# Performance work log

Hardware: AMD Instinct MI355X
Metric: run time of the kernel (lower is better)

## Reference

```python
import jax, jax.numpy as jnp
import numpy as np
import math

# dims
B, DM, H, W = 8, 256, 32, 32
R = 4                      # num_rotations
DI = 2 * DM                # d_inner = expand * d_model = 512
DH = DI // 2               # 256
N = 16                     # d_state
K = 4                      # d_conv
DTR = math.ceil(DM / 16)   # dt_rank = 16


def _dwconv1d(x, w, b):
    # x: (B, C, L); w: (C, 1, K); torch padding='same' (even kernel: extra pad on right)
    lo = (K - 1) // 2
    y = jax.lax.conv_general_dilated(x, w, (1,), [(lo, K - 1 - lo)],
                                     dimension_numbers=('NCH', 'OIH', 'NCH'),
                                     feature_group_count=x.shape[1])
    return y + b[None, :, None]


def _conv2d(x, w, b=None, pad=0):
    y = jax.lax.conv_general_dilated(x, w, (1, 1), [(pad, pad), (pad, pad)],
                                     dimension_numbers=('NCHW', 'OIHW', 'NCHW'))
    return y if b is None else y + b[None, :, None, None]


def _selective_scan(u, delta, A, Bm, Cm):
    # u, delta: (b,r,d,l); A: (r,d,n); Bm, Cm: (b,r,n,l)
    xs = (jnp.moveaxis(delta, -1, 0), jnp.moveaxis(u, -1, 0),
          jnp.moveaxis(Bm, -1, 0), jnp.moveaxis(Cm, -1, 0))
    h0 = jnp.zeros(u.shape[:3] + (A.shape[-1],), u.dtype)  # (b,r,d,n)
    def step(h, inp):
        dt, ut, bt, ct = inp
        h = jnp.exp(dt[..., None] * A) * h + (dt * ut)[..., None] * bt[:, :, None, :]
        return h, jnp.einsum('brdn,brn->brd', h, ct)
    _, ys = jax.lax.scan(step, h0, xs)
    return jnp.moveaxis(ys, 0, -1)  # (b,r,d,l)


def setup_inputs() -> dict:
    key = jax.random.key(0)
    ks = iter(jax.random.split(key, 32))
    def rn(shape, s=0.02):
        return jax.random.normal(next(ks), shape, jnp.float32) * s
    return {
        'x': jax.random.normal(next(ks), (B, DM, H, W), jnp.float32),
        'in_proj_w': rn((DI, DM)),
        'out_proj_w': rn((DM, DI)),
        'conv_x_w': rn((R * DH, 1, K), 0.1), 'conv_x_b': rn((R * DH,), 0.1),
        'conv_z_w': rn((R * DH, 1, K), 0.1), 'conv_z_b': rn((R * DH,), 0.1),
        'x_proj_weight': rn((R, DTR + 2 * N, DH)),
        'dt_projs_weight': jax.random.uniform(next(ks), (R, DH, DTR)) * 0.1,
        'dt_projs_bias': jax.random.uniform(next(ks), (R, DH)) * 0.1,
        'A_logs': jax.random.normal(next(ks), (R * DH, N)) * 0.5,
        'Ds': jnp.ones((R * DH,), jnp.float32),
        'sa_w1': rn((DI // 4, R * DI, 3, 3)), 'sa_b1': jnp.zeros((DI // 4,)),
        'sa_w2': rn((R, DI // 4, 1, 1)), 'sa_b2': jnp.zeros((R,)),
        'ca_w1': rn((DI // 16, R * DI, 1, 1)),
        'ca_w2': rn((R, DI // 16, 1, 1)),
        'gate_w': rn((DI, 2 * DI, 1, 1)), 'gate_b': jnp.zeros((DI,)),
    }


def reference(x, in_proj_w, out_proj_w, conv_x_w, conv_x_b, conv_z_w, conv_z_b,
              x_proj_weight, dt_projs_weight, dt_projs_bias, A_logs, Ds,
              sa_w1, sa_b1, sa_w2, sa_b2, ca_w1, ca_w2, gate_w, gate_b):
    b = x.shape[0]
    L = H * W
    # in_proj (1x1 conv), then 4 rotations (first='l')
    xz = jnp.einsum('bchw,dc->bdhw', x, in_proj_w)                      # (b,DI,H,W)
    xz_rot = jnp.stack([jnp.rot90(xz, r, axes=(2, 3)) for r in range(R)], axis=1)
    xh, zh = jnp.split(xz_rot, 2, axis=2)                               # (b,R,DH,H,W)
    x_seq = jax.nn.silu(_dwconv1d(xh.reshape(b, R * DH, L), conv_x_w, conv_x_b))
    z_seq = jax.nn.silu(_dwconv1d(zh.reshape(b, R * DH, L), conv_z_w, conv_z_b))
    x4 = x_seq.reshape(b, R, DH, L)
    # input-dependent SSM params
    x_dbl = jnp.einsum('brdl,rkd->brkl', x4, x_proj_weight)
    dts, Bm, Cm = jnp.split(x_dbl, [DTR, DTR + N], axis=2)
    delta = jnp.einsum('brkl,rdk->brdl', dts, dt_projs_weight)
    delta = jax.nn.softplus(delta + dt_projs_bias[None, :, :, None])
    A = -jnp.exp(A_logs).reshape(R, DH, N)
    y = _selective_scan(x4, delta, A, Bm, Cm)
    y = y + Ds.reshape(R, DH)[None, :, :, None] * x4
    # MambaVision-style: concat scan output with gated z branch -> d_inner
    y = jnp.concatenate([y, z_seq.reshape(b, R, DH, L)], axis=2).reshape(b, R, DI, H, W)
    # undo rotations so branches are spatially aligned
    y = jnp.stack([jnp.rot90(y[:, r], -r, axes=(2, 3)) for r in range(R)], axis=1)
    # hybrid RotationAwareFusion
    y_flat = y.reshape(b, R * DI, H, W)
    sw = jax.nn.relu(_conv2d(y_flat, sa_w1, sa_b1, pad=1))
    sw = jax.nn.softmax(_conv2d(sw, sa_w2, sa_b2), axis=1)              # (b,R,H,W)
    spatial = jnp.einsum('brchw,brhw->bchw', y, sw)
    cavg = y.mean(axis=(3, 4)).reshape(b, R * DI, 1, 1)
    cw = jax.nn.relu(_conv2d(cavg, ca_w1))
    cw = jax.nn.softmax(_conv2d(cw, ca_w2), axis=1)[:, :, 0, 0]         # (b,R)
    channel = jnp.einsum('brchw,br->bchw', y, cw)
    g = jax.nn.sigmoid(_conv2d(jnp.concatenate([spatial, channel], axis=1), gate_w, gate_b))
    fused = g * spatial + (1.0 - g) * channel                           # (b,DI,H,W)
    out = jnp.einsum('bdhw,cd->bchw', fused, out_proj_w)
    return jax.nn.gelu(out)
```

## Files before the change

kernel.cpp:

```cpp
#include <hip/hip_runtime.h>
#include <math.h>


typedef _Float16 half8 __attribute__((ext_vector_type(8)));
typedef float f4 __attribute__((ext_vector_type(4)));

__device__ __forceinline__ int srcmap(int r, int l) {
  int i = l >> 5, j = l & 31;
  int h, w;
  if (r == 0)      { h = i;      w = j;      }
  else if (r == 1) { h = j;      w = 31 - i; }
  else if (r == 2) { h = 31 - i; w = 31 - j; }
  else             { h = 31 - j; w = i;      }
  return (h << 5) + w;
}

__device__ __forceinline__ float siluf(float x)    { return x / (1.f + __expf(-x)); }
__device__ __forceinline__ float sigmoidf_(float x){ return 1.f / (1.f + __expf(-x)); }
__device__ __forceinline__ float geluf(float x) {
  float x3 = x * x * x;
  return 0.5f * x * (1.f + tanhf(0.7978845608028654f * (x + 0.044715f * x3)));
}

__global__ void k_prep(const float* __restrict__ inw, const float* __restrict__ gw,
                       const float* __restrict__ opw,
                       float* __restrict__ inWT, _Float16* __restrict__ gwH,
                       _Float16* __restrict__ opH) {
  int idx = blockIdx.x * 256 + threadIdx.x;
  if (idx < 131072) {
    int c = idx >> 9, d = idx & 511;
    inWT[idx] = inw[d * 256 + c];
  } else if (idx < 655360) {
    int i = idx - 131072;
    gwH[i] = (_Float16)gw[i];
  } else {
    int i = idx - 655360;
    opH[i] = (_Float16)opw[i];
  }
}

__global__ void k_wprep(const float* __restrict__ saw1, _Float16* __restrict__ Whg2) {
  int o = blockIdx.x * 256 + threadIdx.x;
  int ci = o & 2047;
  int co = (o >> 11) & 127;
  int tap = o >> 18;
  size_t dst = (((size_t)(tap * 64 + (ci >> 5)) * 128) + co) * 32 + (ci & 31);
  Whg2[dst] = (_Float16)saw1[((size_t)co * 2048 + ci) * 9 + tap];
}

__global__ void __launch_bounds__(512) k_inproj(const float* __restrict__ x,
                                                const float* __restrict__ inWT,
                                                float* __restrict__ xz) {
  int d = threadIdx.x;
  int b = blockIdx.y;
  int p0 = blockIdx.x * 16;
  const float* xb = x + (size_t)(b * 256) * 1024 + p0;
  float acc[16];
#pragma unroll
  for (int j = 0; j < 16; ++j) acc[j] = 0.f;
  for (int c = 0; c < 256; ++c) {
    float w = inWT[c * 512 + d];
    const float* xr = xb + c * 1024;
#pragma unroll
    for (int q = 0; q < 4; ++q) {
      float4 v = *(const float4*)(xr + q * 4);
      acc[q*4+0] = fmaf(w, v.x, acc[q*4+0]);
      acc[q*4+1] = fmaf(w, v.y, acc[q*4+1]);
      acc[q*4+2] = fmaf(w, v.z, acc[q*4+2]);
      acc[q*4+3] = fmaf(w, v.w, acc[q*4+3]);
    }
  }
  float* o = xz + (size_t)(b * 512 + d) * 1024 + p0;
#pragma unroll
  for (int q = 0; q < 4; ++q) {
    float4 ov = {acc[q*4+0], acc[q*4+1], acc[q*4+2], acc[q*4+3]};
    *(float4*)(o + q * 4) = ov;
  }
}

__global__ void __launch_bounds__(256) k_conv(const float* __restrict__ xz,
                                              const float* __restrict__ cxw,
                                              const float* __restrict__ cxb,
                                              const float* __restrict__ czw,
                                              const float* __restrict__ czb,
                                              float* __restrict__ xseq,
                                              float* __restrict__ Y) {
  int d = blockIdx.x;
  int b = blockIdx.y;
  __shared__ float xs_t[1024];
  __shared__ float zs_t[1024];
  int t4 = threadIdx.x * 4;
  *(float4*)&xs_t[t4] = *(const float4*)(xz + ((size_t)(b * 512 + d)) * 1024 + t4);
  *(float4*)&zs_t[t4] = *(const float4*)(xz + ((size_t)(b * 512 + 256 + d)) * 1024 + t4);
  __syncthreads();
#pragma unroll
  for (int r = 0; r < 4; ++r) {
    int rd = r * 256 + d;
    float xw0 = cxw[rd*4+0], xw1 = cxw[rd*4+1], xw2 = cxw[rd*4+2], xw3 = cxw[rd*4+3];
    float zw0 = czw[rd*4+0], zw1 = czw[rd*4+1], zw2 = czw[rd*4+2], zw3 = czw[rd*4+3];
    float xbi = cxb[rd], zbi = czb[rd];
    float xo[4], zo[4];
#pragma unroll
    for (int q = 0; q < 4; ++q) {
      int l = t4 + q;
      float ax = xbi, az = zbi;
      if (l - 1 >= 0) {
        int s = srcmap(r, l - 1);
        ax = fmaf(xw0, xs_t[s], ax); az = fmaf(zw0, zs_t[s], az);
      }
      {
        int s = srcmap(r, l);
        ax = fmaf(xw1, xs_t[s], ax); az = fmaf(zw1, zs_t[s], az);
      }
      if (l + 1 < 1024) {
        int s = srcmap(r, l + 1);
        ax = fmaf(xw2, xs_t[s], ax); az = fmaf(zw2, zs_t[s], az);
      }
      if (l + 2 < 1024) {
        int s = srcmap(r, l + 2);
        ax = fmaf(xw3, xs_t[s], ax); az = fmaf(zw3, zs_t[s], az);
      }
      xo[q] = siluf(ax); zo[q] = siluf(az);
    }
    *(float4*)(xseq + ((size_t)(b * 4 + r) * 256 + d) * 1024 + t4) = *(float4*)xo;
    *(float4*)(Y + ((size_t)(b * 4 + r) * 512 + 256 + d) * 1024 + t4) = *(float4*)zo;
  }
}

__global__ void __launch_bounds__(256) k_xdblT(const float* __restrict__ xseq,
                                               const float* __restrict__ xpw,
                                               float* __restrict__ xdT) {
  int ch = blockIdx.x;
  int br = blockIdx.y;
  int r  = br & 3;
  __shared__ float xs_t[256][33];
  const float* base = xseq + (size_t)(br * 256) * 1024 + ch * 32;
  {
    int c4 = threadIdx.x & 7;
    int drow = threadIdx.x >> 3;
#pragma unroll
    for (int p = 0; p < 8; ++p) {
      int dd = p * 32 + drow;
      float4 v = *(const float4*)(base + (size_t)dd * 1024 + c4 * 4);
      xs_t[dd][c4*4+0] = v.x; xs_t[dd][c4*4+1] = v.y;
      xs_t[dd][c4*4+2] = v.z; xs_t[dd][c4*4+3] = v.w;
    }
  }
  __syncthreads();
  int c  = threadIdx.x & 31;
  int kq = threadIdx.x >> 5;
  const float* w = xpw + (r * 48 + kq * 6) * 256;
  float acc[6] = {0.f, 0.f, 0.f, 0.f, 0.f, 0.f};
  for (int d0 = 0; d0 < 256; d0 += 4) {
    float x0 = xs_t[d0][c], x1 = xs_t[d0+1][c], x2 = xs_t[d0+2][c], x3 = xs_t[d0+3][c];
#pragma unroll
    for (int j = 0; j < 6; ++j) {
      float4 wv = *(const float4*)(w + j * 256 + d0);
      acc[j] = fmaf(wv.x, x0, fmaf(wv.y, x1, fmaf(wv.z, x2, fmaf(wv.w, x3, acc[j]))));
    }
  }
  float* o = xdT + ((size_t)(br * 32 + ch) * 32 + c) * 48 + kq * 6;
#pragma unroll
  for (int j = 0; j < 6; ++j) o[j] = acc[j];
}

__global__ void __launch_bounds__(256) k_scanA(
    const float* __restrict__ xseq, const float* __restrict__ xdT,
    const float* __restrict__ dtw_, const float* __restrict__ dtb_,
    const float* __restrict__ alogs,
    float* __restrict__ aprodg, float* __restrict__ Yc) {
  int ch = blockIdx.x;
  int br = blockIdx.y; int r = br & 3;
  int d  = threadIdx.x;
  int rd = r * 256 + d;
  f4 w0 = *(const f4*)&dtw_[rd * 16], w1 = *(const f4*)&dtw_[rd * 16 + 4],
     w2 = *(const f4*)&dtw_[rd * 16 + 8], w3 = *(const f4*)&dtw_[rd * 16 + 12];
  float A2[16], h[16], ap[16];
#pragma unroll
  for (int n = 0; n < 16; ++n) A2[n] = -__expf(alogs[rd * 16 + n]) * 1.44269504f;
#pragma unroll
  for (int n = 0; n < 16; ++n) { h[n] = 0.f; ap[n] = 1.f; }
  float bias = dtb_[rd];
  __shared__ __align__(16) float t2[1536];
  const float* xd = xdT + (size_t)(br * 32 + ch) * 1536;
  for (int i = threadIdx.x; i < 384; i += 256) ((f4*)t2)[i] = ((const f4*)xd)[i];
  __syncthreads();
  const float* us = xseq + (size_t)(br * 256 + d) * 1024 + ch * 32;
  for (int c4 = 0; c4 < 8; ++c4) {
    float4 uv = *(const float4*)(us + c4 * 4);
    float uarr[4] = {uv.x, uv.y, uv.z, uv.w};
#pragma unroll
    for (int cc = 0; cc < 4; ++cc) {
      const f4* row = (const f4*)&t2[(c4 * 4 + cc) * 48];
      f4 td0 = row[0], td1 = row[1], td2 = row[2], td3 = row[3];
      float delta = bias
        + td0[0]*w0[0] + td0[1]*w0[1] + td0[2]*w0[2] + td0[3]*w0[3]
        + td1[0]*w1[0] + td1[1]*w1[1] + td1[2]*w1[2] + td1[3]*w1[3]
        + td2[0]*w2[0] + td2[1]*w2[1] + td2[2]*w2[2] + td2[3]*w2[3]
        + td3[0]*w3[0] + td3[1]*w3[1] + td3[2]*w3[2] + td3[3]*w3[3];
      float sp = (delta > 20.f) ? delta : __logf(1.f + __expf(delta));
      float du = sp * uarr[cc];
      f4 tb[4] = {row[4], row[5], row[6], row[7]};
#pragma unroll
      for (int n = 0; n < 16; ++n) {
        float e = exp2f(sp * A2[n]);
        h[n] = fmaf(e, h[n], du * tb[n >> 2][n & 3]);
        ap[n] *= e;
      }
    }
  }
  float* apo = aprodg + ((size_t)(br * 32 + ch) * 256 + d) * 16;
  float* hco = Yc + (size_t)(br * 512 + d) * 1024 + ch * 32;
#pragma unroll
  for (int n = 0; n < 16; ++n) { apo[n] = ap[n]; hco[n] = h[n]; }
}

__global__ void k_scanB(const float* __restrict__ aprodg, float* __restrict__ Yc) {
  int t  = blockIdx.x * 256 + threadIdx.x;
  int br = t >> 12;
  int dn = t & 4095;
  int d = dn >> 4, n = dn & 15;
  float h = 0.f;
  for (int c = 0; c < 32; ++c) {
    size_t ao = (size_t)(br * 32 + c) * 4096 + dn;
    size_t yo = (size_t)(br * 512 + d) * 1024 + c * 32 + n;
    float hin = h;
    h = fmaf(aprodg[ao], h, Yc[yo]);
    Yc[yo] = hin;
  }
}

__global__ void __launch_bounds__(256) k_scanC(
    const float* __restrict__ xseq, const float* __restrict__ xdT,
    const float* __restrict__ dtw_, const float* __restrict__ dtb_,
    const float* __restrict__ alogs, const float* __restrict__ ds_,
    float* __restrict__ Y) {
  int ch = blockIdx.x;
  int br = blockIdx.y; int r = br & 3;
  int d  = threadIdx.x;
  int rd = r * 256 + d;
  f4 w0 = *(const f4*)&dtw_[rd * 16], w1 = *(const f4*)&dtw_[rd * 16 + 4],
     w2 = *(const f4*)&dtw_[rd * 16 + 8], w3 = *(const f4*)&dtw_[rd * 16 + 12];
  float A2[16], h[16];
#pragma unroll
  for (int n = 0; n < 16; ++n) A2[n] = -__expf(alogs[rd * 16 + n]) * 1.44269504f;
  float bias = dtb_[rd];
  float dsv  = ds_[rd];
  __shared__ __align__(16) float t2[1536];
  __shared__ float yt[32][257];
  const float* xd = xdT + (size_t)(br * 32 + ch) * 1536;
  for (int i = threadIdx.x; i < 384; i += 256) ((f4*)t2)[i] = ((const f4*)xd)[i];
  float* ybase = Y + (size_t)(br * 512 + d) * 1024 + ch * 32;
#pragma unroll
  for (int n = 0; n < 16; ++n) h[n] = ybase[n];
  __syncthreads();
  const float* us = xseq + (size_t)(br * 256 + d) * 1024 + ch * 32;
  for (int c4 = 0; c4 < 8; ++c4) {
    float4 uv = *(const float4*)(us + c4 * 4);
    float uarr[4] = {uv.x, uv.y, uv.z, uv.w};
#pragma unroll
    for (int cc = 0; cc < 4; ++cc) {
      int c = c4 * 4 + cc;
      const f4* row = (const f4*)&t2[c * 48];
      f4 td0 = row[0], td1 = row[1], td2 = row[2], td3 = row[3];
      float delta = bias
        + td0[0]*w0[0] + td0[1]*w0[1] + td0[2]*w0[2] + td0[3]*w0[3]
        + td1[0]*w1[0] + td1[1]*w1[1] + td1[2]*w1[2] + td1[3]*w1[3]
        + td2[0]*w2[0] + td2[1]*w2[1] + td2[2]*w2[2] + td2[3]*w2[3]
        + td3[0]*w3[0] + td3[1]*w3[1] + td3[2]*w3[2] + td3[3]*w3[3];
      float sp = (delta > 20.f) ? delta : __logf(1.f + __expf(delta));
      float du = sp * uarr[cc];
      f4 tb[4] = {row[4], row[5], row[6], row[7]};
      f4 tc[4] = {row[8], row[9], row[10], row[11]};
      float acc = 0.f;
#pragma unroll
      for (int n = 0; n < 16; ++n) {
        float e = exp2f(sp * A2[n]);
        h[n] = fmaf(e, h[n], du * tb[n >> 2][n & 3]);
        acc  = fmaf(h[n], tc[n >> 2][n & 3], acc);
      }
      yt[c][d] = fmaf(dsv, uarr[cc], acc);
    }
  }
  __syncthreads();
  for (int i = threadIdx.x; i < 2048; i += 256) {
    int dd = i >> 3, lq = i & 7;
    f4 v = {yt[lq * 4 + 0][dd], yt[lq * 4 + 1][dd], yt[lq * 4 + 2][dd], yt[lq * 4 + 3][dd]};
    *(f4*)(Y + (size_t)(br * 512 + dd) * 1024 + ch * 32 + lq * 4) = v;
  }
}

__global__ void k_ytr(const float* __restrict__ Y, _Float16* __restrict__ Ytg) {
  __shared__ float t[32][132];
  int l0  = blockIdx.x * 128;
  int ci0 = blockIdx.y * 32;
  int b   = blockIdx.z;
  int r   = ci0 >> 9;
  const float* src = Y + ((size_t)(b * 2048 + ci0)) * 1024 + l0;
#pragma unroll
  for (int i = 0; i < 16; ++i) {
    int idx = threadIdx.x + i * 256;
    int ci = idx >> 7, pp = idx & 127;
    t[ci][pp] = src[(size_t)ci * 1024 + pp];
  }
  __syncthreads();
  int pp = threadIdx.x >> 1;
  int ch = (threadIdx.x & 1) * 16;
  _Float16 buf[16];
#pragma unroll
  for (int j = 0; j < 16; ++j) buf[j] = (_Float16)t[ch + j][pp];
  int pix = srcmap(r, l0 + pp);
  _Float16* dst = Ytg + ((size_t)(b * 1024) + pix) * 2048 + ci0 + ch;
  *(float4*)dst = *(const float4*)buf;
  *(float4*)(dst + 8) = *(const float4*)(buf + 8);
}

__global__ void __launch_bounds__(256, 2) k_samfma(const _Float16* __restrict__ Ytg,
                                                   const _Float16* __restrict__ Whg2,
                                                   float* __restrict__ cpart) {
  __shared__ __align__(16) _Float16 As[6][32][40];
  __shared__ __align__(16) _Float16 Bs[9][64][40];
  int L = blockIdx.x;
  int ks = L & 7;
  int rem = L >> 3;
  int b = rem >> 3, rg = rem & 7;
  int tid = threadIdx.x;
  int wid = tid >> 6, lane = tid & 63;
  int r = lane & 15, g = lane >> 4;
  const _Float16* Yb = Ytg + (size_t)b * (1024 * 2048);
  const half8 zero8 = {0, 0, 0, 0, 0, 0, 0, 0};

  int srow[3], scol[3], sci8[3], srcoff[3]; bool sok[3];
#pragma unroll
  for (int i = 0; i < 3; ++i) {
    int unit = tid + i * 256;
    srow[i] = unit >> 7; scol[i] = (unit >> 2) & 31; sci8[i] = unit & 3;
    int grow = rg * 4 - 1 + srow[i];
    sok[i] = ((unsigned)grow < 32u);
    srcoff[i] = ((sok[i] ? grow : 0) * 32 + scol[i]) * 2048 + sci8[i] * 8;
  }
  int bcol = tid >> 2, bci8 = tid & 3;
  int ci_base = ks * 256;

  for (int coh = 0; coh < 2; ++coh) {
    f4 acc[2][4];
#pragma unroll
    for (int mi = 0; mi < 2; ++mi)
#pragma unroll
      for (int ni = 0; ni < 4; ++ni) acc[mi][ni] = (f4){0.f, 0.f, 0.f, 0.f};

    half8 pa[3], pb[9];
#pragma unroll
    for (int i = 0; i < 3; ++i) {
      half8 v = *(const half8*)(Yb + srcoff[i] + ci_base);
      pa[i] = sok[i] ? v : zero8;
    }
#pragma unroll
    for (int j = 0; j < 9; ++j)
      pb[j] = *(const half8*)(Whg2 + (((size_t)(j * 64 + ks * 8) * 128) + coh * 64 + bcol) * 32 + bci8 * 8);

    for (int ch = 0; ch < 8; ++ch) {
      __syncthreads();
#pragma unroll
      for (int i = 0; i < 3; ++i)
        *(half8*)&As[srow[i]][scol[i]][sci8[i] * 8] = pa[i];
#pragma unroll
      for (int j = 0; j < 9; ++j)
        *(half8*)&Bs[j][bcol][bci8 * 8] = pb[j];
      if (ch < 7) {
        int ci0 = ci_base + (ch + 1) * 32;
#pragma unroll
        for (int i = 0; i < 3; ++i) {
          half8 v = *(const half8*)(Yb + srcoff[i] + ci0);
          pa[i] = sok[i] ? v : zero8;
        }
        int cic = ks * 8 + ch + 1;
#pragma unroll
        for (int j = 0; j < 9; ++j)
          pb[j] = *(const half8*)(Whg2 + (((size_t)(j * 64 + cic) * 128) + coh * 64 + bcol) * 32 + bci8 * 8);
      }
      __syncthreads();

#pragma unroll
      for (int tap = 0; tap < 9; ++tap) {
        const int dh = tap / 3 - 1, dw = tap % 3 - 1;
        int lrow = wid + dh + 1;
        half8 av[2], bv[4];
#pragma unroll
        for (int mi = 0; mi < 2; ++mi) {
          int lcol = mi * 16 + r + dw;
          bool ok = ((unsigned)lcol < 32u);
          half8 v = *(const half8*)&As[lrow][lcol & 31][g * 8];
          av[mi] = ok ? v : zero8;
        }
#pragma unroll
        for (int ni = 0; ni < 4; ++ni)
          bv[ni] = *(const half8*)&Bs[tap][ni * 16 + r][g * 8];
#pragma unroll
        for (int mi = 0; mi < 2; ++mi)
#pragma unroll
          for (int ni = 0; ni < 4; ++ni)
            acc[mi][ni] = __builtin_amdgcn_mfma_f32_16x16x32_f16(av[mi], bv[ni], acc[mi][ni], 0, 0, 0);
      }
    }

    float* cp = cpart + (size_t)ks * (8192 * 128);
    int basepix = b * 1024 + (rg * 4 + wid) * 32;
#pragma unroll
    for (int mi = 0; mi < 2; ++mi)
#pragma unroll
      for (int ni = 0; ni < 4; ++ni) {
        int co = coh * 64 + ni * 16 + r;
#pragma unroll
        for (int j = 0; j < 4; ++j)
          cp[(size_t)(basepix + mi * 16 + g * 4 + j) * 128 + co] = acc[mi][ni][j];
      }
    __syncthreads();
  }
}

__global__ void __launch_bounds__(256) k_saconv2f(const float* __restrict__ cpart,
                                                  const float* __restrict__ sab1,
                                                  const float* __restrict__ saw2,
                                                  const float* __restrict__ sab2,
                                                  float* __restrict__ swout) {
  int tid = threadIdx.x;
  int pixg = tid >> 3, cig = tid & 7;
  int p = blockIdx.x * 32 + pixg;
  int b = blockIdx.y;
  int pix = b * 1024 + p;
  const float* c0 = cpart + (size_t)pix * 128 + cig * 16;
  float a0 = 0.f, a1 = 0.f, a2 = 0.f, a3 = 0.f;
#pragma unroll
  for (int j4 = 0; j4 < 4; ++j4) {
    float sx = 0.f, sy = 0.f, sz = 0.f, sw_ = 0.f;
#pragma unroll
    for (int k = 0; k < 8; ++k) {
      float4 v = *(const float4*)(c0 + (size_t)k * 1048576 + j4 * 4);
      sx += v.x; sy += v.y; sz += v.z; sw_ += v.w;
    }
    int ci = cig * 16 + j4 * 4;
    float v0 = fmaxf(sx + sab1[ci],     0.f);
    float v1 = fmaxf(sy + sab1[ci + 1], 0.f);
    float v2 = fmaxf(sz + sab1[ci + 2], 0.f);
    float v3 = fmaxf(sw_ + sab1[ci + 3], 0.f);
    a0 = fmaf(v0, saw2[ci], fmaf(v1, saw2[ci+1], fmaf(v2, saw2[ci+2], fmaf(v3, saw2[ci+3], a0))));
    a1 = fmaf(v0, saw2[128+ci], fmaf(v1, saw2[128+ci+1], fmaf(v2, saw2[128+ci+2], fmaf(v3, saw2[128+ci+3], a1))));
    a2 = fmaf(v0, saw2[256+ci], fmaf(v1, saw2[256+ci+1], fmaf(v2, saw2[256+ci+2], fmaf(v3, saw2[256+ci+3], a2))));
    a3 = fmaf(v0, saw2[384+ci], fmaf(v1, saw2[384+ci+1], fmaf(v2, saw2[384+ci+2], fmaf(v3, saw2[384+ci+3], a3))));
  }
#pragma unroll
  for (int off = 4; off > 0; off >>= 1) {
    a0 += __shfl_down(a0, off, 8);
    a1 += __shfl_down(a1, off, 8);
    a2 += __shfl_down(a2, off, 8);
    a3 += __shfl_down(a3, off, 8);
  }
  if (cig == 0) {
    a0 += sab2[0]; a1 += sab2[1]; a2 += sab2[2]; a3 += sab2[3];
    float m = fmaxf(fmaxf(a0, a1), fmaxf(a2, a3));
    float e0 = __expf(a0 - m), e1 = __expf(a1 - m), e2 = __expf(a2 - m), e3 = __expf(a3 - m);
    float inv = 1.f / (e0 + e1 + e2 + e3);
    swout[(b * 4 + 0) * 1024 + p] = e0 * inv;
    swout[(b * 4 + 1) * 1024 + p] = e1 * inv;
    swout[(b * 4 + 2) * 1024 + p] = e2 * inv;
    swout[(b * 4 + 3) * 1024 + p] = e3 * inv;
  }
}

__global__ void k_cavg(const float* __restrict__ Y, float* __restrict__ cavg) {
  int gidq = blockIdx.x * 256 + threadIdx.x;
  int row = gidq >> 2, q = gidq & 3;
  const float4* yr = (const float4*)(Y + (size_t)row * 1024 + q * 256);
  float s = 0.f;
  for (int i = 0; i < 64; ++i) {
    float4 v = yr[i];
    s += v.x + v.y + v.z + v.w;
  }
  s += __shfl_down(s, 2, 4);
  s += __shfl_down(s, 1, 4);
  if (q == 0) cavg[row] = s * (1.f / 1024.f);
}

__global__ void k_cw(const float* __restrict__ cavg, const float* __restrict__ caw1,
                     const float* __restrict__ caw2, float* __restrict__ cwout) {
  int b = blockIdx.x;
  int t = threadIdx.x;
  __shared__ float hid[32];
  __shared__ float vv[4];
  if (t < 32) {
    float a = 0.f;
    const float* cv = cavg + b * 2048;
    const float* wr = caw1 + t * 2048;
    for (int i = 0; i < 2048; ++i) a = fmaf(wr[i], cv[i], a);
    hid[t] = fmaxf(a, 0.f);
  }
  __syncthreads();
  if (t < 4) {
    float a = 0.f;
    for (int i = 0; i < 32; ++i) a = fmaf(caw2[t * 32 + i], hid[i], a);
    vv[t] = a;
  }
  __syncthreads();
  if (t < 4) {
    float m = fmaxf(fmaxf(vv[0], vv[1]), fmaxf(vv[2], vv[3]));
    float e = __expf(vv[t] - m);
    float s = __expf(vv[0] - m) + __expf(vv[1] - m) + __expf(vv[2] - m) + __expf(vv[3] - m);
    cwout[b * 4 + t] = e / s;
  }
}

__global__ void __launch_bounds__(256) k_catH(const _Float16* __restrict__ Ytg,
                                              const float* __restrict__ swv,
                                              const float* __restrict__ cwv,
                                              _Float16* __restrict__ catO) {
  int p0 = blockIdx.x * 64, c0 = blockIdx.y * 64, b = blockIdx.z;
  int pp = threadIdx.x >> 2, cs = (threadIdx.x & 3) * 16;
  int pix = p0 + pp;
  const _Float16* src = Ytg + (size_t)(b * 1024 + pix) * 2048 + c0 + cs;
  float accS[16], accC[16];
#pragma unroll
  for (int j = 0; j < 16; ++j) { accS[j] = 0.f; accC[j] = 0.f; }
#pragma unroll
  for (int r = 0; r < 4; ++r) {
    half8 v0 = *(const half8*)(src + r * 512);
    half8 v1 = *(const half8*)(src + r * 512 + 8);
    float sw = swv[(size_t)(b * 4 + r) * 1024 + pix];
    float cw = cwv[b * 4 + r];
#pragma unroll
    for (int j = 0; j < 8; ++j) {
      float f0 = (float)v0[j], f1 = (float)v1[j];
      accS[j]     = fmaf(f0, sw, accS[j]);
      accS[j + 8] = fmaf(f1, sw, accS[j + 8]);
      accC[j]     = fmaf(f0, cw, accC[j]);
      accC[j + 8] = fmaf(f1, cw, accC[j + 8]);
    }
  }
  _Float16 os[16], oc[16];
#pragma unroll
  for (int j = 0; j < 16; ++j) { os[j] = (_Float16)accS[j]; oc[j] = (_Float16)accC[j]; }
  _Float16* dst = catO + ((size_t)(b * 1024) + pix) * 1024;
  *(half8*)(dst + c0 + cs)       = *(half8*)os;
  *(half8*)(dst + c0 + cs + 8)   = *(half8*)(os + 8);
  *(half8*)(dst + 512 + c0 + cs)     = *(half8*)oc;
  *(half8*)(dst + 512 + c0 + cs + 8) = *(half8*)(oc + 8);
}

__global__ void __launch_bounds__(256) k_gatemfma(const _Float16* __restrict__ catO,
                                                  const _Float16* __restrict__ gwH,
                                                  const float* __restrict__ gb,
                                                  _Float16* __restrict__ fusedH) {
  int wid = threadIdx.x >> 6, lane = threadIdx.x & 63;
  int r = lane & 15, g = lane >> 4;
  int p0 = blockIdx.x * 128 + (wid >> 1) * 64;
  int c0 = blockIdx.y * 128 + (wid & 1) * 64;
  int b  = blockIdx.z;
  const _Float16* Cb = catO + (size_t)b * (1024 * 1024);
  f4 acc[4][4];
#pragma unroll
  for (int mi = 0; mi < 4; ++mi)
#pragma unroll
    for (int ni = 0; ni < 4; ++ni) acc[mi][ni] = (f4){0.f, 0.f, 0.f, 0.f};
  for (int kk = 0; kk < 1024; kk += 32) {
    half8 av[4], bv[4];
#pragma unroll
    for (int mi = 0; mi < 4; ++mi)
      av[mi] = *(const half8*)(Cb + (size_t)(p0 + mi * 16 + r) * 1024 + kk + g * 8);
#pragma unroll
    for (int ni = 0; ni < 4; ++ni)
      bv[ni] = *(const half8*)(gwH + (size_t)(c0 + ni * 16 + r) * 1024 + kk + g * 8);
#pragma unroll
    for (int mi = 0; mi < 4; ++mi)
#pragma unroll
      for (int ni = 0; ni < 4; ++ni)
        acc[mi][ni] = __builtin_amdgcn_mfma_f32_16x16x32_f16(av[mi], bv[ni], acc[mi][ni], 0, 0, 0);
  }
#pragma unroll
  for (int ni = 0; ni < 4; ++ni) {
    int c = c0 + ni * 16 + r;
    float bias = gb[c];
#pragma unroll
    for (int mi = 0; mi < 4; ++mi)
#pragma unroll
      for (int j = 0; j < 4; ++j) {
        int pix = p0 + mi * 16 + g * 4 + j;
        const _Float16* rowp = Cb + (size_t)pix * 1024 + c;
        float sp = (float)rowp[0], ch = (float)rowp[512];
        float gt = sigmoidf_(acc[mi][ni][j] + bias);
        fusedH[((size_t)(b * 1024) + pix) * 512 + c] = (_Float16)(gt * sp + (1.f - gt) * ch);
      }
  }
}

__global__ void __launch_bounds__(256) k_outprojmfma(const _Float16* __restrict__ fusedH,
                                                     const _Float16* __restrict__ opH,
                                                     float* __restrict__ out) {
  int wid = threadIdx.x >> 6, lane = threadIdx.x & 63;
  int r = lane & 15, g = lane >> 4;
  int m0 = blockIdx.x * 64;
  int n0 = blockIdx.y * 256 + wid * 64;
  int b  = blockIdx.z;
  f4 acc[4][4];
#pragma unroll
  for (int mi = 0; mi < 4; ++mi)
#pragma unroll
    for (int ni = 0; ni < 4; ++ni) acc[mi][ni] = (f4){0.f, 0.f, 0.f, 0.f};
  for (int kk = 0; kk < 512; kk += 32) {
    half8 av[4], bv[4];
#pragma unroll
    for (int mi = 0; mi < 4; ++mi)
      av[mi] = *(const half8*)(opH + (size_t)(m0 + mi * 16 + r) * 512 + kk + g * 8);
#pragma unroll
    for (int ni = 0; ni < 4; ++ni)
      bv[ni] = *(const half8*)(fusedH + ((size_t)(b * 1024) + n0 + ni * 16 + r) * 512 + kk + g * 8);
#pragma unroll
    for (int mi = 0; mi < 4; ++mi)
#pragma unroll
      for (int ni = 0; ni < 4; ++ni)
        acc[mi][ni] = __builtin_amdgcn_mfma_f32_16x16x32_f16(av[mi], bv[ni], acc[mi][ni], 0, 0, 0);
  }
#pragma unroll
  for (int mi = 0; mi < 4; ++mi)
#pragma unroll
    for (int ni = 0; ni < 4; ++ni) {
      int pix = n0 + ni * 16 + r;
#pragma unroll
      for (int j = 0; j < 4; ++j) {
        int co = m0 + mi * 16 + g * 4 + j;
        out[((size_t)(b * 256) + co) * 1024 + pix] = geluf(acc[mi][ni][j]);
      }
    }
}

extern "C" void kernel_launch(void* const* d_in, const int* in_sizes, int n_in,
                              void* d_out, int out_size, void* d_ws, size_t ws_size,
                              hipStream_t stream) {
  const float* x    = (const float*)d_in[0];
  const float* inw  = (const float*)d_in[1];
  const float* opw  = (const float*)d_in[2];
  const float* cxw  = (const float*)d_in[3];
  const float* cxb  = (const float*)d_in[4];
  const float* czw  = (const float*)d_in[5];
  const float* czb  = (const float*)d_in[6];
  const float* xpw  = (const float*)d_in[7];
  const float* dtw  = (const float*)d_in[8];
  const float* dtb  = (const float*)d_in[9];
  const float* alog = (const float*)d_in[10];
  const float* ds   = (const float*)d_in[11];
  const float* saw1 = (const float*)d_in[12];
  const float* sab1 = (const float*)d_in[13];
  const float* saw2 = (const float*)d_in[14];
  const float* sab2 = (const float*)d_in[15];
  const float* caw1 = (const float*)d_in[16];
  const float* caw2 = (const float*)d_in[17];
  const float* gw   = (const float*)d_in[18];
  const float* gb   = (const float*)d_in[19];

  float* ws = (float*)d_ws;
  float* xz   = ws + 0;
  float* xseq = ws + 4194304;
  float* xdT  = ws + 12582912;
  float* Y    = ws + 14155776;
  float* swb  = ws + 31981568;
  float* cavg = ws + 32014336;
  float* cwb  = ws + 32030720;
  float* inWT = ws + 32030752;
  float* opHF = ws + 32161824;
  float* gwHF = ws + 32292896;
  float* WhgF = ws + 32817184;
  float* aprodg = xz;
  float* Cpart  = Y;
  _Float16* Ytg    = (_Float16*)xseq;
  _Float16* catO   = (_Float16*)xz;
  _Float16* fusedH = (_Float16*)xseq;
  _Float16* Whg2 = (_Float16*)WhgF;
  _Float16* gwH = (_Float16*)gwHF;
  _Float16* opH = (_Float16*)opHF;

  k_prep<<<3072, 256, 0, stream>>>(inw, gw, opw, inWT, gwH, opH);
  k_wprep<<<9216, 256, 0, stream>>>(saw1, Whg2);
  k_inproj<<<dim3(64, 8), 512, 0, stream>>>(x, inWT, xz);
  k_conv<<<dim3(256, 8), 256, 0, stream>>>(xz, cxw, cxb, czw, czb, xseq, Y);
  k_xdblT<<<dim3(32, 32), 256, 0, stream>>>(xseq, xpw, xdT);
  k_scanA<<<dim3(32, 32), 256, 0, stream>>>(xseq, xdT, dtw, dtb, alog, aprodg, Y);
  k_scanB<<<512, 256, 0, stream>>>(aprodg, Y);
  k_scanC<<<dim3(32, 32), 256, 0, stream>>>(xseq, xdT, dtw, dtb, alog, ds, Y);
  k_ytr<<<dim3(8, 64, 8), 256, 0, stream>>>(Y, Ytg);
  k_cavg<<<256, 256, 0, stream>>>(Y, cavg);
  k_cw<<<8, 64, 0, stream>>>(cavg, caw1, caw2, cwb);
  k_samfma<<<512, 256, 0, stream>>>(Ytg, Whg2, Cpart);
  k_saconv2f<<<dim3(32, 8), 256, 0, stream>>>(Cpart, sab1, saw2, sab2, swb);
  k_catH<<<dim3(16, 8, 8), 256, 0, stream>>>(Ytg, swb, cwb, catO);
  k_gatemfma<<<dim3(8, 4, 8), 256, 0, stream>>>(catO, gwH, gb, fusedH);
  k_outprojmfma<<<dim3(4, 4, 8), 256, 0, stream>>>(fusedH, opH, (float*)d_out);
}
```

Measured before the change: 454.2 us.

## Move in-projection to split-fp16 MFMA and compute chunk decay from summed dt

Replaces the scalar FP32 in-projection with a transpose kernel that splits x into high and low fp16 halves, followed by an MFMA GEMM. The GEMM uses three products (hh, hl, lh) to keep near-fp32 accuracy while running on matrix cores. Separately, the scan's per-chunk decay product is now computed as exp2 of the summed dt times A, which removes 16 multiplies per step. The cost is an extra transpose pass, a temporary buffer aliased into Y, and a small difference in rounding.

```diff
diff --git a/kernel.cpp b/kernel.cpp
--- a/kernel.cpp
+++ b/kernel.cpp
@@ -24,12 +24,14 @@
 
 __global__ void k_prep(const float* __restrict__ inw, const float* __restrict__ gw,
                        const float* __restrict__ opw,
-                       float* __restrict__ inWT, _Float16* __restrict__ gwH,
-                       _Float16* __restrict__ opH) {
+                       _Float16* __restrict__ inwH, _Float16* __restrict__ inwL,
+                       _Float16* __restrict__ gwH, _Float16* __restrict__ opH) {
   int idx = blockIdx.x * 256 + threadIdx.x;
   if (idx < 131072) {
-    int c = idx >> 9, d = idx & 511;
-    inWT[idx] = inw[d * 256 + c];
+    float v = inw[idx];
+    _Float16 h = (_Float16)v;
+    inwH[idx] = h;
+    inwL[idx] = (_Float16)(v - (float)h);
   } else if (idx < 655360) {
     int i = idx - 131072;
     gwH[i] = (_Float16)gw[i];
@@ -48,34 +50,85 @@
   Whg2[dst] = (_Float16)saw1[((size_t)co * 2048 + ci) * 9 + tap];
 }
 
-__global__ void __launch_bounds__(512) k_inproj(const float* __restrict__ x,
-                                                const float* __restrict__ inWT,
-                                                float* __restrict__ xz) {
-  int d = threadIdx.x;
-  int b = blockIdx.y;
-  int p0 = blockIdx.x * 16;
-  const float* xb = x + (size_t)(b * 256) * 1024 + p0;
-  float acc[16];
-#pragma unroll
-  for (int j = 0; j < 16; ++j) acc[j] = 0.f;
-  for (int c = 0; c < 256; ++c) {
-    float w = inWT[c * 512 + d];
-    const float* xr = xb + c * 1024;
-#pragma unroll
-    for (int q = 0; q < 4; ++q) {
-      float4 v = *(const float4*)(xr + q * 4);
-      acc[q*4+0] = fmaf(w, v.x, acc[q*4+0]);
-      acc[q*4+1] = fmaf(w, v.y, acc[q*4+1]);
-      acc[q*4+2] = fmaf(w, v.z, acc[q*4+2]);
-      acc[q*4+3] = fmaf(w, v.w, acc[q*4+3]);
-    }
-  }
-  float* o = xz + (size_t)(b * 512 + d) * 1024 + p0;
-#pragma unroll
-  for (int q = 0; q < 4; ++q) {
-    float4 ov = {acc[q*4+0], acc[q*4+1], acc[q*4+2], acc[q*4+3]};
-    *(float4*)(o + q * 4) = ov;
-  }
+__global__ void __launch_bounds__(256) k_xT(const float* __restrict__ x,
+                                            _Float16* __restrict__ xTh,
+                                            _Float16* __restrict__ xTl) {
+  __shared__ float t[32][132];
+  int p0 = blockIdx.x * 128, c0 = blockIdx.y * 32, b = blockIdx.z;
+  const float* src = x + ((size_t)(b * 256 + c0)) * 1024 + p0;
+#pragma unroll
+  for (int i = 0; i < 16; ++i) {
+    int idx = threadIdx.x + i * 256;
+    int ci = idx >> 7, pp = idx & 127;
+    t[ci][pp] = src[(size_t)ci * 1024 + pp];
+  }
+  __syncthreads();
+  int pp = threadIdx.x >> 1;
+  int ch = (threadIdx.x & 1) * 16;
+  _Float16 bh[16], bl[16];
+#pragma unroll
+  for (int j = 0; j < 16; ++j) {
+    float f = t[ch + j][pp];
+    _Float16 h = (_Float16)f;
+    bh[j] = h;
+    bl[j] = (_Float16)(f - (float)h);
+  }
+  size_t o = ((size_t)(b * 1024) + p0 + pp) * 256 + c0 + ch;
+  *(half8*)(xTh + o)     = *(half8*)bh;
+  *(half8*)(xTh + o + 8) = *(half8*)(bh + 8);
+  *(half8*)(xTl + o)     = *(half8*)bl;
+  *(half8*)(xTl + o + 8) = *(half8*)(bl + 8);
+}
+
+__global__ void __launch_bounds__(256) k_inprojmfma(const _Float16* __restrict__ xTh,
+                                                    const _Float16* __restrict__ xTl,
+                                                    const _Float16* __restrict__ inwH,
+                                                    const _Float16* __restrict__ inwL,
+                                                    float* __restrict__ xz) {
+  int wid = threadIdx.x >> 6, lane = threadIdx.x & 63;
+  int r = lane & 15, g = lane >> 4;
+  int m0 = blockIdx.x * 128 + (wid >> 1) * 64;
+  int n0 = blockIdx.y * 128 + (wid & 1) * 64;
+  int b  = blockIdx.z;
+  f4 acc[4][4];
+#pragma unroll
+  for (int mi = 0; mi < 4; ++mi)
+#pragma unroll
+    for (int ni = 0; ni < 4; ++ni) acc[mi][ni] = (f4){0.f, 0.f, 0.f, 0.f};
+  for (int kk = 0; kk < 256; kk += 32) {
+    half8 ah[4], al[4], bh[4], bl[4];
+#pragma unroll
+    for (int mi = 0; mi < 4; ++mi) {
+      size_t o = (size_t)(m0 + mi * 16 + r) * 256 + kk + g * 8;
+      ah[mi] = *(const half8*)(inwH + o);
+      al[mi] = *(const half8*)(inwL + o);
+    }
+#pragma unroll
+    for (int ni = 0; ni < 4; ++ni) {
+      size_t o = ((size_t)(b * 1024) + n0 + ni * 16 + r) * 256 + kk + g * 8;
+      bh[ni] = *(const half8*)(xTh + o);
+      bl[ni] = *(const half8*)(xTl + o);
+    }
+#pragma unroll
+    for (int mi = 0; mi < 4; ++mi)
+#pragma unroll
+      for (int ni = 0; ni < 4; ++ni) {
+        acc[mi][ni] = __builtin_amdgcn_mfma_f32_16x16x32_f16(ah[mi], bh[ni], acc[mi][ni], 0, 0, 0);
+        acc[mi][ni] = __builtin_amdgcn_mfma_f32_16x16x32_f16(ah[mi], bl[ni], acc[mi][ni], 0, 0, 0);
+        acc[mi][ni] = __builtin_amdgcn_mfma_f32_16x16x32_f16(al[mi], bh[ni], acc[mi][ni], 0, 0, 0);
+      }
+  }
+#pragma unroll
+  for (int mi = 0; mi < 4; ++mi)
+#pragma unroll
+    for (int ni = 0; ni < 4; ++ni) {
+      int pix = n0 + ni * 16 + r;
+#pragma unroll
+      for (int j = 0; j < 4; ++j) {
+        int d = m0 + mi * 16 + g * 4 + j;
+        xz[((size_t)(b * 512) + d) * 1024 + pix] = acc[mi][ni][j];
+      }
+    }
 }
 
 __global__ void __launch_bounds__(256) k_conv(const float* __restrict__ xz,
@@ -175,11 +228,12 @@
   int rd = r * 256 + d;
   f4 w0 = *(const f4*)&dtw_[rd * 16], w1 = *(const f4*)&dtw_[rd * 16 + 4],
      w2 = *(const f4*)&dtw_[rd * 16 + 8], w3 = *(const f4*)&dtw_[rd * 16 + 12];
-  float A2[16], h[16], ap[16];
+  float A2[16], h[16];
 #pragma unroll
   for (int n = 0; n < 16; ++n) A2[n] = -__expf(alogs[rd * 16 + n]) * 1.44269504f;
 #pragma unroll
-  for (int n = 0; n < 16; ++n) { h[n] = 0.f; ap[n] = 1.f; }
+  for (int n = 0; n < 16; ++n) h[n] = 0.f;
+  float spsum = 0.f;
   float bias = dtb_[rd];
   __shared__ __align__(16) float t2[1536];
   const float* xd = xdT + (size_t)(br * 32 + ch) * 1536;
@@ -200,19 +254,19 @@
         + td3[0]*w3[0] + td3[1]*w3[1] + td3[2]*w3[2] + td3[3]*w3[3];
       float sp = (delta > 20.f) ? delta : __logf(1.f + __expf(delta));
       float du = sp * uarr[cc];
+      spsum += sp;
       f4 tb[4] = {row[4], row[5], row[6], row[7]};
 #pragma unroll
       for (int n = 0; n < 16; ++n) {
         float e = exp2f(sp * A2[n]);
         h[n] = fmaf(e, h[n], du * tb[n >> 2][n & 3]);
-        ap[n] *= e;
       }
     }
   }
   float* apo = aprodg + ((size_t)(br * 32 + ch) * 256 + d) * 16;
   float* hco = Yc + (size_t)(br * 512 + d) * 1024 + ch * 32;
 #pragma unroll
-  for (int n = 0; n < 16; ++n) { apo[n] = ap[n]; hco[n] = h[n]; }
+  for (int n = 0; n < 16; ++n) { apo[n] = exp2f(spsum * A2[n]); hco[n] = h[n]; }
 }
 
 __global__ void k_scanB(const float* __restrict__ aprodg, float* __restrict__ Yc) {
@@ -664,7 +718,7 @@
   float* swb  = ws + 31981568;
   float* cavg = ws + 32014336;
   float* cwb  = ws + 32030720;
-  float* inWT = ws + 32030752;
+  float* inWHL= ws + 32030752;
   float* opHF = ws + 32161824;
   float* gwHF = ws + 32292896;
   float* WhgF = ws + 32817184;
@@ -676,10 +730,15 @@
   _Float16* Whg2 = (_Float16*)WhgF;
   _Float16* gwH = (_Float16*)gwHF;
   _Float16* opH = (_Float16*)opHF;
-
-  k_prep<<<3072, 256, 0, stream>>>(inw, gw, opw, inWT, gwH, opH);
+  _Float16* inwH = (_Float16*)inWHL;
+  _Float16* inwL = (_Float16*)(inWHL + 65536);
+  _Float16* xTh  = (_Float16*)Y;
+  _Float16* xTl  = (_Float16*)(Y + 1048576);
+
+  k_prep<<<3072, 256, 0, stream>>>(inw, gw, opw, inwH, inwL, gwH, opH);
   k_wprep<<<9216, 256, 0, stream>>>(saw1, Whg2);
-  k_inproj<<<dim3(64, 8), 512, 0, stream>>>(x, inWT, xz);
+  k_xT<<<dim3(8, 8, 8), 256, 0, stream>>>(x, xTh, xTl);
+  k_inprojmfma<<<dim3(4, 8, 8), 256, 0, stream>>>(xTh, xTl, inwH, inwL, xz);
   k_conv<<<dim3(256, 8), 256, 0, stream>>>(xz, cxw, cxb, czw, czb, xseq, Y);
   k_xdblT<<<dim3(32, 32), 256, 0, stream>>>(xseq, xpw, xdT);
   k_scanA<<<dim3(32, 32), 256, 0, stream>>>(xseq, xdT, dtw, dtb, alog, aprodg, Y);
```

Result: faster. 439.9 us (-3.2%).
